# Performance work log

Hardware: AMD Instinct MI355X
Metric: run time of the kernel (lower is better)

Reference implementation:

```python
import jax, jax.numpy as jnp
import numpy as np

N = 50000      # nodes
E = 1600000    # edges
L = 128        # latent_size


def _mlp(h, W1, b1, W2, b2):
    # MLP(in_dim, [L, L]) == Linear -> ReLU -> Linear
    return jax.nn.relu(h @ W1 + b1) @ W2 + b2


def setup_inputs() -> dict:
    key = jax.random.key(0)
    ks = jax.random.split(key, 12)
    glorot = lambda k, i, o: jax.random.normal(k, (i, o), jnp.float32) * (2.0 / (i + o)) ** 0.5
    return {
        "pos": jax.random.normal(ks[0], (N, 3), jnp.float32),
        "x": jax.random.normal(ks[1], (N, L), jnp.float32),
        "edge_attr": jax.random.normal(ks[2], (E, L), jnp.float32),
        "edge_index": jax.random.randint(ks[3], (2, E), 0, N, jnp.int64),
        "last_pred": jax.random.normal(ks[4], (N, 3), jnp.float32),
        "mask_idx": jax.random.randint(ks[5], (N, 1), 0, 2, jnp.int32).astype(bool),
        # pos_embedding MLP params (in=3)
        "Wp1": glorot(ks[6], 3, L), "bp1": jnp.zeros((L,), jnp.float32),
        "Wp2": glorot(ks[7], L, L), "bp2": jnp.zeros((L,), jnp.float32),
        # dis_embedding MLP params (in=1)
        "Wd1": glorot(ks[8], 1, L), "bd1": jnp.zeros((L,), jnp.float32),
        "Wd2": glorot(ks[9], L, L), "bd2": jnp.zeros((L,), jnp.float32),
    }


def reference(pos, x, edge_attr, edge_index, last_pred, mask_idx,
              Wp1, bp1, Wp2, bp2, Wd1, bd1, Wd2, bd2):
    # mode == 'mask': replace masked node positions with last prediction
    pos = jnp.where(mask_idx, last_pred, pos)                    # [N,3]
    extended_x = x + _mlp(pos, Wp1, bp1, Wp2, bp2)               # [N,L]
    row, col = edge_index[0], edge_index[1]
    diff = pos[row] - pos[col]                                   # [E,3]
    length = jnp.linalg.norm(diff, axis=-1, keepdims=True)       # [E,1]
    extended_edge_attr = edge_attr + _mlp(length, Wd1, bd1, Wd2, bd2)  # [E,L]
    return extended_x, extended_edge_attr
```

## Files before the change

### kernel.cpp

```cpp
#include <hip/hip_runtime.h>
#include <hip/hip_bf16.h>

#define NN 50000
#define EE 1600000
#define NT_E 12500
#define NT_TOT 12891

typedef float f32x4 __attribute__((ext_vector_type(4)));
typedef __bf16 bf16x8 __attribute__((ext_vector_type(8)));

__device__ __forceinline__ float edge_len(int e, const int* __restrict__ eidx,
                                          const float* __restrict__ pos,
                                          const float* __restrict__ lp,
                                          const int* __restrict__ msk) {
    int ri = eidx[e];
    int ci = eidx[EE + e];
    const float* pr = msk[ri] ? lp : pos;
    const float* pc = msk[ci] ? lp : pos;
    float dx = pr[3 * ri + 0] - pc[3 * ci + 0];
    float dy = pr[3 * ri + 1] - pc[3 * ci + 1];
    float dz = pr[3 * ri + 2] - pc[3 * ci + 2];
    return sqrtf(dx * dx + dy * dy + dz * dz);
}

__global__ __launch_bounds__(256) void len_kernel(
    const int* __restrict__ eidx, const float* __restrict__ pos,
    const float* __restrict__ lp, const int* __restrict__ msk,
    float* __restrict__ len)
{
    int e = blockIdx.x * 256 + threadIdx.x;
    if (e < EE) len[e] = edge_len(e, eidx, pos, lp, msk);
}

__device__ __forceinline__ void stage_w2(const float* __restrict__ W2, __bf16* w2l) {
    for (int idx = threadIdx.x; idx < 128 * 128; idx += 512) {
        int k = idx >> 7;
        int c = idx & 127;
        int dst = (((k >> 5) * 8 + (c >> 4)) * 64 + (((k >> 3) & 3) * 16 + (c & 15))) * 8 + (k & 7);
        w2l[dst] = (__bf16)W2[idx];
    }
}

template <bool PRECOMP>
__global__ __launch_bounds__(512, 3) void fused_kernel(
    const float* __restrict__ pos, const float* __restrict__ x,
    const float* __restrict__ ea, const int* __restrict__ eidx,
    const float* __restrict__ lp, const int* __restrict__ msk,
    const float* __restrict__ Wp1, const float* __restrict__ bp1,
    const float* __restrict__ Wp2, const float* __restrict__ bp2,
    const float* __restrict__ Wd1, const float* __restrict__ bd1,
    const float* __restrict__ Wd2, const float* __restrict__ bd2,
    const float* __restrict__ len,
    float* __restrict__ outx, float* __restrict__ oute)
{
    __shared__ __bf16 w2l[16384];
    __shared__ float w1l[384], b1l[128], b2l[128];
    __shared__ float tbuf[8][512];

    stage_w2(Wd2, w2l);
    if (threadIdx.x < 128) {
        w1l[threadIdx.x] = Wd1[threadIdx.x];
        b1l[threadIdx.x] = bd1[threadIdx.x];
        b2l[threadIdx.x] = bd2[threadIdx.x];
    }
    __syncthreads();

    const int w = threadIdx.x >> 6;
    const int l = threadIdx.x & 63;
    const int llo = l & 15;
    const int lgrp = l >> 4;
    float* tb = tbuf[w];

    bool node_staged = false;

    for (int t = blockIdx.x; t < NT_TOT; t += gridDim.x) {
        const bool is_edge = (t < NT_E);
        if (!is_edge && !node_staged) {
            __syncthreads();
            stage_w2(Wp2, w2l);
            for (int i = threadIdx.x; i < 384; i += 512) w1l[i] = Wp1[i];
            if (threadIdx.x < 128) {
                b1l[threadIdx.x] = bp1[threadIdx.x];
                b2l[threadIdx.x] = bp2[threadIdx.x];
            }
            __syncthreads();
            node_staged = true;
        }

        const int base = is_edge ? t * 128 : (t - NT_E) * 128;
        const int e0 = base + w * 16;
        const bool valid = is_edge || (e0 + 16 <= NN);

        f32x4 ear[8];
        f32x4 acc[8];
        if (valid) {
            const float* srow = (is_edge ? ea : x) + (size_t)e0 * 128;
#pragma unroll
            for (int j = 0; j < 8; j++) ear[j] = *(const f32x4*)(srow + j * 256 + l * 4);

            float lenv = 0.f, px = 0.f, py = 0.f, pz = 0.f;
            if (is_edge) {
                lenv = PRECOMP ? len[e0 + llo] : edge_len(e0 + llo, eidx, pos, lp, msk);
            } else {
                int nd = e0 + llo;
                const float* p = msk[nd] ? lp : pos;
                px = p[3 * nd + 0];
                py = p[3 * nd + 1];
                pz = p[3 * nd + 2];
            }

#pragma unroll
            for (int m = 0; m < 8; m++) acc[m] = (f32x4){0.f, 0.f, 0.f, 0.f};

#pragma unroll
            for (int kk = 0; kk < 4; kk++) {
                bf16x8 hf;
#pragma unroll
                for (int j = 0; j < 8; j++) {
                    int k = kk * 32 + lgrp * 8 + j;
                    float h = is_edge
                        ? lenv * w1l[k] + b1l[k]
                        : px * w1l[k] + py * w1l[128 + k] + pz * w1l[256 + k] + b1l[k];
                    hf[j] = (__bf16)fmaxf(h, 0.f);
                }
#pragma unroll
                for (int m = 0; m < 8; m++) {
                    bf16x8 wf = *(const bf16x8*)&w2l[((kk * 8 + m) * 64 + l) * 8];
                    acc[m] = __builtin_amdgcn_mfma_f32_16x16x32_bf16(wf, hf, acc[m], 0, 0, 0);
                }
            }
        }

        float* drow = (is_edge ? oute : outx) + (size_t)e0 * 128;
        f32x4 b2v = *(const f32x4*)&b2l[(l & 31) * 4];

#pragma unroll
        for (int p = 0; p < 4; p++) {
            if (valid && (llo >> 2) == p) {
                int r = llo & 3;
#pragma unroll
                for (int m = 0; m < 8; m++) {
                    int c = (m * 16 + lgrp * 4 + r * 4) & 127;
                    *(f32x4*)&tb[r * 128 + c] = acc[m];
                }
            }
            __syncthreads();
            if (valid) {
#pragma unroll
                for (int i = 0; i < 2; i++) {
                    int row = 2 * i + (l >> 5);
                    int c = ((l & 31) * 4 + row * 4) & 127;
                    f32x4 tv = *(const f32x4*)&tb[row * 128 + c];
                    f32x4 o = tv + b2v + ear[p * 2 + i];
                    *(f32x4*)(drow + p * 512 + i * 256 + l * 4) = o;
                }
            }
            __syncthreads();
        }
    }
}

extern "C" void kernel_launch(void* const* d_in, const int* in_sizes, int n_in,
                              void* d_out, int out_size, void* d_ws, size_t ws_size,
                              hipStream_t stream) {
    const float* pos        = (const float*)d_in[0];
    const float* x          = (const float*)d_in[1];
    const float* edge_attr  = (const float*)d_in[2];
    const int* edge_index   = (const int*)d_in[3];
    const float* last_pred  = (const float*)d_in[4];
    const int* mask         = (const int*)d_in[5];
    const float* Wp1 = (const float*)d_in[6];
    const float* bp1 = (const float*)d_in[7];
    const float* Wp2 = (const float*)d_in[8];
    const float* bp2 = (const float*)d_in[9];
    const float* Wd1 = (const float*)d_in[10];
    const float* bd1 = (const float*)d_in[11];
    const float* Wd2 = (const float*)d_in[12];
    const float* bd2 = (const float*)d_in[13];

    float* outx = (float*)d_out;
    float* oute = outx + (size_t)NN * 128;
    float* len  = (float*)d_ws;

    if (ws_size >= (size_t)EE * sizeof(float)) {
        len_kernel<<<(EE + 255) / 256, 256, 0, stream>>>(edge_index, pos, last_pred, mask, len);
        fused_kernel<true><<<768, 512, 0, stream>>>(
            pos, x, edge_attr, edge_index, last_pred, mask,
            Wp1, bp1, Wp2, bp2, Wd1, bd1, Wd2, bd2, len, outx, oute);
    } else {
        fused_kernel<false><<<768, 512, 0, stream>>>(
            pos, x, edge_attr, edge_index, last_pred, mask,
            Wp1, bp1, Wp2, bp2, Wd1, bd1, Wd2, bd2, len, outx, oute);
    }
}
```

Measured before the change: 397.4 us.

## Replace edge MLP with piecewise-linear lookup over sorted ReLU breakpoints

The edge MLP has a scalar input, so its output is piecewise linear in the length. Two small prep kernels sort the ReLU breakpoints and precompute a slope and intercept table, 129 intervals by 128 channels. A streaming edge kernel then binary-searches each length's interval and computes ea + len*A + B with nontemporal loads and stores, dropping the per-edge MFMA GEMM. The node MLP moves into its own kernel. This adds four extra launches and changes numerics from bf16 matmul to fp32 exact-form evaluation.

```diff
diff --git a/kernel.cpp b/kernel.cpp
--- a/kernel.cpp
+++ b/kernel.cpp
@@ -3,11 +3,16 @@
 
 #define NN 50000
 #define EE 1600000
-#define NT_E 12500
-#define NT_TOT 12891
+#define NT_N 391
+#define NIV 129
 
 typedef float f32x4 __attribute__((ext_vector_type(4)));
 typedef __bf16 bf16x8 __attribute__((ext_vector_type(8)));
+
+__device__ float gT[128];
+__device__ int   gRank[128];
+__device__ __align__(16) float gA[NIV * 128];
+__device__ __align__(16) float gB[NIV * 128];
 
 __device__ __forceinline__ float edge_len(int e, const int* __restrict__ eidx,
                                           const float* __restrict__ pos,
@@ -23,6 +28,40 @@
     return sqrtf(dx * dx + dy * dy + dz * dz);
 }
 
+__global__ void prep1(const float* __restrict__ Wd1, const float* __restrict__ bd1) {
+    int k = threadIdx.x;
+    float w1 = Wd1[k], b1 = bd1[k];
+    float t = (w1 == 0.f) ? __builtin_inff() : (-b1 / w1);
+    int rank = 0;
+    for (int j = 0; j < 128; j++) {
+        float w1j = Wd1[j], b1j = bd1[j];
+        float tj = (w1j == 0.f) ? __builtin_inff() : (-b1j / w1j);
+        rank += (tj < t) || (tj == t && j < k);
+    }
+    gRank[k] = rank;
+    gT[rank] = t;
+}
+
+__global__ void prep2(const float* __restrict__ Wd1, const float* __restrict__ bd1,
+                      const float* __restrict__ Wd2, const float* __restrict__ bd2) {
+    int i = blockIdx.x;
+    int c = threadIdx.x;
+    float a = 0.f, b = 0.f;
+    for (int k = 0; k < 128; k++) {
+        float w1 = Wd1[k], b1 = bd1[k];
+        bool act = (w1 > 0.f) ? (gRank[k] < i)
+                 : (w1 < 0.f) ? (gRank[k] >= i)
+                              : (b1 > 0.f);
+        if (act) {
+            float w2 = Wd2[k * 128 + c];
+            a = fmaf(w1, w2, a);
+            b = fmaf(b1, w2, b);
+        }
+    }
+    gA[i * 128 + c] = a;
+    gB[i * 128 + c] = b + bd2[c];
+}
+
 __global__ __launch_bounds__(256) void len_kernel(
     const int* __restrict__ eidx, const float* __restrict__ pos,
     const float* __restrict__ lp, const int* __restrict__ msk,
@@ -32,6 +71,39 @@
     if (e < EE) len[e] = edge_len(e, eidx, pos, lp, msk);
 }
 
+template <bool PRECOMP>
+__global__ __launch_bounds__(256) void edge_kernel(
+    const float* __restrict__ ea, const float* __restrict__ len,
+    const int* __restrict__ eidx, const float* __restrict__ pos,
+    const float* __restrict__ lp, const int* __restrict__ msk,
+    float* __restrict__ oute)
+{
+    __shared__ float ts[128];
+    if (threadIdx.x < 128) ts[threadIdx.x] = gT[threadIdx.x];
+    __syncthreads();
+
+    const int g  = threadIdx.x >> 5;
+    const int c4 = (threadIdx.x & 31) * 4;
+
+    for (int r = blockIdx.x * 8 + g; r < EE; r += gridDim.x * 8) {
+        float lv = PRECOMP ? len[r] : edge_len(r, eidx, pos, lp, msk);
+
+        int lo = 0;
+#pragma unroll
+        for (int s = 128; s > 0; s >>= 1) {
+            int m = lo + s;
+            if (m <= 128 && ts[m - 1] < lv) lo = m;
+        }
+
+        const f32x4 a = *(const f32x4*)&gA[lo * 128 + c4];
+        const f32x4 b = *(const f32x4*)&gB[lo * 128 + c4];
+        const size_t off = (size_t)r * 128 + c4;
+        f32x4 e = __builtin_nontemporal_load((const f32x4*)(ea + off));
+        f32x4 o = e + (lv * a + b);
+        __builtin_nontemporal_store(o, (f32x4*)(oute + off));
+    }
+}
+
 __device__ __forceinline__ void stage_w2(const float* __restrict__ W2, __bf16* w2l) {
     for (int idx = threadIdx.x; idx < 128 * 128; idx += 512) {
         int k = idx >> 7;
@@ -41,27 +113,22 @@
     }
 }
 
-template <bool PRECOMP>
-__global__ __launch_bounds__(512, 3) void fused_kernel(
+__global__ __launch_bounds__(512, 3) void node_kernel(
     const float* __restrict__ pos, const float* __restrict__ x,
-    const float* __restrict__ ea, const int* __restrict__ eidx,
     const float* __restrict__ lp, const int* __restrict__ msk,
     const float* __restrict__ Wp1, const float* __restrict__ bp1,
     const float* __restrict__ Wp2, const float* __restrict__ bp2,
-    const float* __restrict__ Wd1, const float* __restrict__ bd1,
-    const float* __restrict__ Wd2, const float* __restrict__ bd2,
-    const float* __restrict__ len,
-    float* __restrict__ outx, float* __restrict__ oute)
+    float* __restrict__ outx)
 {
     __shared__ __bf16 w2l[16384];
     __shared__ float w1l[384], b1l[128], b2l[128];
     __shared__ float tbuf[8][512];
 
-    stage_w2(Wd2, w2l);
+    stage_w2(Wp2, w2l);
+    for (int i = threadIdx.x; i < 384; i += 512) w1l[i] = Wp1[i];
     if (threadIdx.x < 128) {
-        w1l[threadIdx.x] = Wd1[threadIdx.x];
-        b1l[threadIdx.x] = bd1[threadIdx.x];
-        b2l[threadIdx.x] = bd2[threadIdx.x];
+        b1l[threadIdx.x] = bp1[threadIdx.x];
+        b2l[threadIdx.x] = bp2[threadIdx.x];
     }
     __syncthreads();
 
@@ -71,92 +138,68 @@
     const int lgrp = l >> 4;
     float* tb = tbuf[w];
 
-    bool node_staged = false;
-
-    for (int t = blockIdx.x; t < NT_TOT; t += gridDim.x) {
-        const bool is_edge = (t < NT_E);
-        if (!is_edge && !node_staged) {
-            __syncthreads();
-            stage_w2(Wp2, w2l);
-            for (int i = threadIdx.x; i < 384; i += 512) w1l[i] = Wp1[i];
-            if (threadIdx.x < 128) {
-                b1l[threadIdx.x] = bp1[threadIdx.x];
-                b2l[threadIdx.x] = bp2[threadIdx.x];
-            }
-            __syncthreads();
-            node_staged = true;
-        }
-
-        const int base = is_edge ? t * 128 : (t - NT_E) * 128;
-        const int e0 = base + w * 16;
-        const bool valid = is_edge || (e0 + 16 <= NN);
-
-        f32x4 ear[8];
-        f32x4 acc[8];
+    const int base = blockIdx.x * 128;
+    const int e0 = base + w * 16;
+    const bool valid = (e0 + 16 <= NN);
+
+    f32x4 ear[8];
+    f32x4 acc[8];
+    if (valid) {
+        const float* srow = x + (size_t)e0 * 128;
+#pragma unroll
+        for (int j = 0; j < 8; j++) ear[j] = *(const f32x4*)(srow + j * 256 + l * 4);
+
+        int nd = e0 + llo;
+        const float* p = msk[nd] ? lp : pos;
+        float px = p[3 * nd + 0];
+        float py = p[3 * nd + 1];
+        float pz = p[3 * nd + 2];
+
+#pragma unroll
+        for (int m = 0; m < 8; m++) acc[m] = (f32x4){0.f, 0.f, 0.f, 0.f};
+
+#pragma unroll
+        for (int kk = 0; kk < 4; kk++) {
+            bf16x8 hf;
+#pragma unroll
+            for (int j = 0; j < 8; j++) {
+                int k = kk * 32 + lgrp * 8 + j;
+                float h = px * w1l[k] + py * w1l[128 + k] + pz * w1l[256 + k] + b1l[k];
+                hf[j] = (__bf16)fmaxf(h, 0.f);
+            }
+#pragma unroll
+            for (int m = 0; m < 8; m++) {
+                bf16x8 wf = *(const bf16x8*)&w2l[((kk * 8 + m) * 64 + l) * 8];
+                acc[m] = __builtin_amdgcn_mfma_f32_16x16x32_bf16(wf, hf, acc[m], 0, 0, 0);
+            }
+        }
+    }
+
+    float* drow = outx + (size_t)e0 * 128;
+    f32x4 b2v = *(const f32x4*)&b2l[(l & 31) * 4];
+
+#pragma unroll
+    for (int p = 0; p < 4; p++) {
+        if (valid && (llo >> 2) == p) {
+            int r = llo & 3;
+#pragma unroll
+            for (int m = 0; m < 8; m++) {
+                int c = (m * 16 + lgrp * 4 + r * 4) & 127;
+                *(f32x4*)&tb[r * 128 + c] = acc[m];
+            }
+        }
+        __syncthreads();
         if (valid) {
-            const float* srow = (is_edge ? ea : x) + (size_t)e0 * 128;
-#pragma unroll
-            for (int j = 0; j < 8; j++) ear[j] = *(const f32x4*)(srow + j * 256 + l * 4);
-
-            float lenv = 0.f, px = 0.f, py = 0.f, pz = 0.f;
-            if (is_edge) {
-                lenv = PRECOMP ? len[e0 + llo] : edge_len(e0 + llo, eidx, pos, lp, msk);
-            } else {
-                int nd = e0 + llo;
-                const float* p = msk[nd] ? lp : pos;
-                px = p[3 * nd + 0];
-                py = p[3 * nd + 1];
-                pz = p[3 * nd + 2];
-            }
-
-#pragma unroll
-            for (int m = 0; m < 8; m++) acc[m] = (f32x4){0.f, 0.f, 0.f, 0.f};
-
-#pragma unroll
-            for (int kk = 0; kk < 4; kk++) {
-                bf16x8 hf;
-#pragma unroll
-                for (int j = 0; j < 8; j++) {
-                    int k = kk * 32 + lgrp * 8 + j;
-                    float h = is_edge
-                        ? lenv * w1l[k] + b1l[k]
-                        : px * w1l[k] + py * w1l[128 + k] + pz * w1l[256 + k] + b1l[k];
-                    hf[j] = (__bf16)fmaxf(h, 0.f);
-                }
-#pragma unroll
-                for (int m = 0; m < 8; m++) {
-                    bf16x8 wf = *(const bf16x8*)&w2l[((kk * 8 + m) * 64 + l) * 8];
-                    acc[m] = __builtin_amdgcn_mfma_f32_16x16x32_bf16(wf, hf, acc[m], 0, 0, 0);
-                }
-            }
-        }
-
-        float* drow = (is_edge ? oute : outx) + (size_t)e0 * 128;
-        f32x4 b2v = *(const f32x4*)&b2l[(l & 31) * 4];
-
-#pragma unroll
-        for (int p = 0; p < 4; p++) {
-            if (valid && (llo >> 2) == p) {
-                int r = llo & 3;
-#pragma unroll
-                for (int m = 0; m < 8; m++) {
-                    int c = (m * 16 + lgrp * 4 + r * 4) & 127;
-                    *(f32x4*)&tb[r * 128 + c] = acc[m];
-                }
-            }
-            __syncthreads();
-            if (valid) {
-#pragma unroll
-                for (int i = 0; i < 2; i++) {
-                    int row = 2 * i + (l >> 5);
-                    int c = ((l & 31) * 4 + row * 4) & 127;
-                    f32x4 tv = *(const f32x4*)&tb[row * 128 + c];
-                    f32x4 o = tv + b2v + ear[p * 2 + i];
-                    *(f32x4*)(drow + p * 512 + i * 256 + l * 4) = o;
-                }
-            }
-            __syncthreads();
-        }
+#pragma unroll
+            for (int i = 0; i < 2; i++) {
+                int row = 2 * i + (l >> 5);
+                int c = ((l & 31) * 4 + row * 4) & 127;
+                f32x4 tv = *(const f32x4*)&tb[row * 128 + c];
+                f32x4 o = tv + b2v + ear[p * 2 + i];
+                *(f32x4*)(drow + p * 512 + i * 256 + l * 4) = o;
+            }
+        }
+        __syncthreads();
     }
 }
 
@@ -182,14 +225,18 @@
     float* oute = outx + (size_t)NN * 128;
     float* len  = (float*)d_ws;
 
+    prep1<<<1, 128, 0, stream>>>(Wd1, bd1);
+    prep2<<<NIV, 128, 0, stream>>>(Wd1, bd1, Wd2, bd2);
+
+    node_kernel<<<NT_N, 512, 0, stream>>>(pos, x, last_pred, mask,
+                                          Wp1, bp1, Wp2, bp2, outx);
+
     if (ws_size >= (size_t)EE * sizeof(float)) {
         len_kernel<<<(EE + 255) / 256, 256, 0, stream>>>(edge_index, pos, last_pred, mask, len);
-        fused_kernel<true><<<768, 512, 0, stream>>>(
-            pos, x, edge_attr, edge_index, last_pred, mask,
-            Wp1, bp1, Wp2, bp2, Wd1, bd1, Wd2, bd2, len, outx, oute);
+        edge_kernel<true><<<2048, 256, 0, stream>>>(edge_attr, len, edge_index,
+                                                    pos, last_pred, mask, oute);
     } else {
-        fused_kernel<false><<<768, 512, 0, stream>>>(
-            pos, x, edge_attr, edge_index, last_pred, mask,
-            Wp1, bp1, Wp2, bp2, Wd1, bd1, Wd2, bd2, len, outx, oute);
-    }
-}
+        edge_kernel<false><<<2048, 256, 0, stream>>>(edge_attr, nullptr, edge_index,
+                                                     pos, last_pred, mask, oute);
+    }
+}
```

Measured after the change: 383.2 us. 1.04x faster.
